# Kernel optimization log

Measured on AMD Instinct MI355X. Metric: run time of the kernel, lower is better.

## Reference

```python
import jax, jax.numpy as jnp
import numpy as np

SEQ, BATCH, IN, HID = 2048, 4096, 4, 3


def setup_inputs() -> dict:
    key = jax.random.key(0)
    ks = jax.random.split(key, 6)
    s = 1.0 / np.sqrt(HID)  # PyTorch RNN init scale
    return {
        "x": jax.random.normal(ks[0], (SEQ, BATCH, IN), dtype=jnp.float32),
        "h0": jax.random.normal(ks[1], (1, BATCH, HID), dtype=jnp.float32),
        "W_ih": jax.random.uniform(ks[2], (HID, IN), minval=-s, maxval=s, dtype=jnp.float32),
        "W_hh": jax.random.uniform(ks[3], (HID, HID), minval=-s, maxval=s, dtype=jnp.float32),
        "b_ih": jax.random.uniform(ks[4], (HID,), minval=-s, maxval=s, dtype=jnp.float32),
        "b_hh": jax.random.uniform(ks[5], (HID,), minval=-s, maxval=s, dtype=jnp.float32),
    }


def reference(x, h0, W_ih, W_hh, b_ih, b_hh):
    # Single-layer ReLU RNN (batch_first=False):
    #   h_t = relu(x_t @ W_ih^T + b_ih + h_{t-1} @ W_hh^T + b_hh)
    # Precompute the input projection for all timesteps (vectorized GEMM),
    # then scan only the tiny recurrent update.
    pre = jnp.einsum('tbi,hi->tbh', x, W_ih) + b_ih + b_hh  # [T,B,H]

    def step(h, pre_t):
        h_new = jax.nn.relu(pre_t + h @ W_hh.T)  # [B,H]
        return h_new, h_new

    h_last, outs = jax.lax.scan(step, h0[0], pre)
    return outs, h_last[None]  # ([T,B,H], [1,B,H]) as nn.RNN returns
```

## Files before the change

kernel.cpp:

```cpp
#include <hip/hip_runtime.h>

#define T_SEQ   2048
#define BATCH   4096
#define BPB     16
#define NBLK    (BATCH / BPB)
#define CHUNK   64
#define NCHUNK  (T_SEQ / CHUNK)
#define XR      4
#define NS      3
#define NITER   (NCHUNK + 1)

typedef float v4f __attribute__((ext_vector_type(4)));

#define AS1c(p) ((const __attribute__((address_space(1))) void*)(p))
#define AS3(p)  ((__attribute__((address_space(3))) void*)(p))

#define BARRIER() do {                              \
    __builtin_amdgcn_sched_barrier(0);              \
    asm volatile("s_barrier" ::: "memory");         \
    __builtin_amdgcn_sched_barrier(0);              \
} while (0)

#define QBCAST(hf, pat) \
    __builtin_bit_cast(float, __builtin_amdgcn_mov_dpp( \
        __builtin_bit_cast(int, (hf)), (pat), 0xF, 0xF, true))

__global__ __launch_bounds__(256, 1) void rnn_fused(
    const float* __restrict__ x,
    const float* __restrict__ h0,
    const float* __restrict__ Wih,
    const float* __restrict__ Whh,
    const float* __restrict__ bih,
    const float* __restrict__ bhh,
    float* __restrict__ out)
{
    __shared__ v4f xs[XR * CHUNK * BPB];

    const int tid  = threadIdx.x;
    const int lane = tid & 63;
    const int wid  = tid >> 6;
    const int b0   = blockIdx.x * BPB;

    if (wid > 0) {
        const int s = wid - 1;
        const v4f* __restrict__ xg = (const v4f*)x;
        const int vlo = (lane >> 4) * BATCH + b0 + (lane & 15);

#define STAGE(c) do {                                                          \
        const int _slot = ((c) & (XR - 1)) * (CHUNK * BPB);                    \
        _Pragma("unroll")                                                      \
        for (int _g = 0; _g < CHUNK / 4; ++_g) {                               \
            __builtin_amdgcn_global_load_lds(                                  \
                AS1c(xg + ((size_t)(c) * CHUNK + _g * 4) * BATCH + vlo),       \
                AS3(&xs[_slot + _g * (4 * BPB)]), 16, 0, 0);                   \
        }                                                                      \
    } while (0)

        if (s == 0) STAGE(0);
        if (s == 1) STAGE(1);
#pragma unroll 1
        for (int i = 0; i < NITER; ++i) {
            const int ci = i + 2;
            if (ci < NCHUNK && (ci % NS) == s) STAGE(ci);
            if (i < NCHUNK && (i % NS) == s)
                asm volatile("s_waitcnt vmcnt(0)" ::: "memory");
            BARRIER();
        }
#undef STAGE
    } else {
        const int bi = lane >> 2;
        const int j  = lane & 3;
        const int jj = (j < 3) ? j : 2;

        const float w0 = Wih[jj * 4 + 0], w1 = Wih[jj * 4 + 1];
        const float w2 = Wih[jj * 4 + 2], w3 = Wih[jj * 4 + 3];
        const float a0 = Whh[jj * 3 + 0], a1 = Whh[jj * 3 + 1];
        const float a2 = Whh[jj * 3 + 2];
        const float bb = bih[jj] + bhh[jj];

        float h = h0[(b0 + bi) * 3 + jj];
        const size_t ooff = (size_t)(b0 + bi) * 3 + j;

#pragma unroll 1
        for (int i = 0; i < NITER; ++i) {
            const int c = i - 1;
            if (c >= 0 && j < 3) {
                const v4f* __restrict__ xr = &xs[(c & (XR - 1)) * (CHUNK * BPB) + bi];
                float* __restrict__ op = out + (size_t)c * CHUNK * (BATCH * 3) + ooff;
#pragma unroll
                for (int tt = 0; tt < CHUNK; ++tt) {
                    v4f xv = xr[tt * BPB];
                    float p = fmaf(w0, xv.x, fmaf(w1, xv.y,
                              fmaf(w2, xv.z, fmaf(w3, xv.w, bb))));
                    float g0 = QBCAST(h, 0x00);
                    float g1 = QBCAST(h, 0x55);
                    float g2 = QBCAST(h, 0xAA);
                    float t0 = fmaf(a0, g0, fmaf(a1, g1, fmaf(a2, g2, p)));
                    h = fmaxf(t0, 0.0f);
                    op[(size_t)tt * (BATCH * 3)] = h;
                }
            }
            BARRIER();
        }
        if (j < 3)
            out[(size_t)T_SEQ * BATCH * 3 + ooff] = h;
    }
}

extern "C" void kernel_launch(void* const* d_in, const int* in_sizes, int n_in,
                              void* d_out, int out_size, void* d_ws, size_t ws_size,
                              hipStream_t stream) {
    const float* x   = (const float*)d_in[0];
    const float* h0  = (const float*)d_in[1];
    const float* Wih = (const float*)d_in[2];
    const float* Whh = (const float*)d_in[3];
    const float* bih = (const float*)d_in[4];
    const float* bhh = (const float*)d_in[5];
    float* out = (float*)d_out;

    rnn_fused<<<NBLK, 256, 0, stream>>>(x, h0, Wih, Whh, bih, bhh, out);
}
```

Measured before the change: 250.7 us.

## Split RNN into projection, recurrence, and store warps with deeper LDS pipeline

Adds a dedicated wavefront that computes the input projection into an LDS buffer, and another that copies recurrent outputs from LDS to global memory with coalesced 16-byte stores. This leaves the serial recurrence wave with only the DPP broadcast, three FMAs and an LDS write per step, with prefetched projection values. The block grows to 384 threads, the pipeline gets two more stages, and more LDS and barriers are used.

```diff
diff --git a/kernel.cpp b/kernel.cpp
--- a/kernel.cpp
+++ b/kernel.cpp
@@ -7,8 +7,10 @@
 #define CHUNK   64
 #define NCHUNK  (T_SEQ / CHUNK)
 #define XR      4
+#define NP      2
+#define NO      2
 #define NS      3
-#define NITER   (NCHUNK + 1)
+#define NITER   (NCHUNK + 3)
 
 typedef float v4f __attribute__((ext_vector_type(4)));
 
@@ -21,11 +23,13 @@
     __builtin_amdgcn_sched_barrier(0);              \
 } while (0)
 
+#define LGKM0() asm volatile("s_waitcnt lgkmcnt(0)" ::: "memory")
+
 #define QBCAST(hf, pat) \
     __builtin_bit_cast(float, __builtin_amdgcn_mov_dpp( \
         __builtin_bit_cast(int, (hf)), (pat), 0xF, 0xF, true))
 
-__global__ __launch_bounds__(256, 1) void rnn_fused(
+__global__ __launch_bounds__(384, 1) void rnn_fused(
     const float* __restrict__ x,
     const float* __restrict__ h0,
     const float* __restrict__ Wih,
@@ -34,25 +38,27 @@
     const float* __restrict__ bhh,
     float* __restrict__ out)
 {
-    __shared__ v4f xs[XR * CHUNK * BPB];
+    __shared__ v4f  xs[XR * CHUNK * BPB];
+    __shared__ v4f  ps[NP * CHUNK * BPB];
+    __shared__ float hs[NO * CHUNK * 48];
 
     const int tid  = threadIdx.x;
     const int lane = tid & 63;
     const int wid  = tid >> 6;
     const int b0   = blockIdx.x * BPB;
 
-    if (wid > 0) {
-        const int s = wid - 1;
+    if (wid >= 2 && wid <= 4) {
+        const int s = wid - 2;
         const v4f* __restrict__ xg = (const v4f*)x;
         const int vlo = (lane >> 4) * BATCH + b0 + (lane & 15);
 
 #define STAGE(c) do {                                                          \
-        const int _slot = ((c) & (XR - 1)) * (CHUNK * BPB);                    \
+        const int _s0 = ((c) & (XR - 1)) * (CHUNK * BPB);                      \
         _Pragma("unroll")                                                      \
         for (int _g = 0; _g < CHUNK / 4; ++_g) {                               \
             __builtin_amdgcn_global_load_lds(                                  \
                 AS1c(xg + ((size_t)(c) * CHUNK + _g * 4) * BATCH + vlo),       \
-                AS3(&xs[_slot + _g * (4 * BPB)]), 16, 0, 0);                   \
+                AS3(&xs[_s0 + _g * (4 * BPB)]), 16, 0, 0);                     \
         }                                                                      \
     } while (0)
 
@@ -67,43 +73,101 @@
             BARRIER();
         }
 #undef STAGE
-    } else {
+    } else if (wid == 1) {
+        const int ts = lane >> 4;
+        const int bi = lane & 15;
+        const float w00 = Wih[0], w01 = Wih[1], w02 = Wih[2],  w03 = Wih[3];
+        const float w10 = Wih[4], w11 = Wih[5], w12 = Wih[6],  w13 = Wih[7];
+        const float w20 = Wih[8], w21 = Wih[9], w22 = Wih[10], w23 = Wih[11];
+        const float bb0 = bih[0] + bhh[0];
+        const float bb1 = bih[1] + bhh[1];
+        const float bb2 = bih[2] + bhh[2];
+#pragma unroll 1
+        for (int i = 0; i < NITER; ++i) {
+            const int c = i - 1;
+            if (c >= 0 && c < NCHUNK) {
+                const v4f* __restrict__ xb = &xs[((c & (XR - 1)) * CHUNK + ts) * BPB + bi];
+                v4f* __restrict__ pw = &ps[((c & (NP - 1)) * CHUNK + ts) * BPB + bi];
+                v4f xa = xb[0];
+                v4f xc = xb[64];
+#pragma unroll
+                for (int g = 0; g < 16; ++g) {
+                    v4f xv = xa; xa = xc;
+                    xc = xb[(g + 2) * 64];
+                    float p0 = fmaf(w00, xv.x, fmaf(w01, xv.y,
+                               fmaf(w02, xv.z, fmaf(w03, xv.w, bb0))));
+                    float p1 = fmaf(w10, xv.x, fmaf(w11, xv.y,
+                               fmaf(w12, xv.z, fmaf(w13, xv.w, bb1))));
+                    float p2 = fmaf(w20, xv.x, fmaf(w21, xv.y,
+                               fmaf(w22, xv.z, fmaf(w23, xv.w, bb2))));
+                    v4f pv; pv.x = p0; pv.y = p1; pv.z = p2; pv.w = p2;
+                    pw[g * 64] = pv;
+                }
+                LGKM0();
+            }
+            BARRIER();
+        }
+    } else if (wid == 0) {
         const int bi = lane >> 2;
         const int j  = lane & 3;
         const int jj = (j < 3) ? j : 2;
-
-        const float w0 = Wih[jj * 4 + 0], w1 = Wih[jj * 4 + 1];
-        const float w2 = Wih[jj * 4 + 2], w3 = Wih[jj * 4 + 3];
-        const float a0 = Whh[jj * 3 + 0], a1 = Whh[jj * 3 + 1];
-        const float a2 = Whh[jj * 3 + 2];
-        const float bb = bih[jj] + bhh[jj];
-
+        const float a0 = Whh[jj * 3 + 0], a1 = Whh[jj * 3 + 1], a2 = Whh[jj * 3 + 2];
         float h = h0[(b0 + bi) * 3 + jj];
-        const size_t ooff = (size_t)(b0 + bi) * 3 + j;
 
 #pragma unroll 1
         for (int i = 0; i < NITER; ++i) {
-            const int c = i - 1;
-            if (c >= 0 && j < 3) {
-                const v4f* __restrict__ xr = &xs[(c & (XR - 1)) * (CHUNK * BPB) + bi];
-                float* __restrict__ op = out + (size_t)c * CHUNK * (BATCH * 3) + ooff;
+            const int c = i - 2;
+            if (c >= 0 && c < NCHUNK && j < 3) {
+                const float* __restrict__ pb =
+                    (const float*)&ps[(c & (NP - 1)) * CHUNK * BPB] + bi * 4 + jj;
+                float* __restrict__ hb = &hs[(c & (NO - 1)) * CHUNK * 48 + bi * 3 + j];
+                float q0 = pb[0 * 64], q1 = pb[1 * 64], q2 = pb[2 * 64], q3 = pb[3 * 64];
+                float q4 = pb[4 * 64], q5 = pb[5 * 64], q6 = pb[6 * 64], q7 = pb[7 * 64];
+#define STEPC(TT, Q) do {                                                      \
+                float g2 = QBCAST(h, 0xAA);                                    \
+                float g1 = QBCAST(h, 0x55);                                    \
+                float g0 = QBCAST(h, 0x00);                                    \
+                float t0 = fmaf(a0, g0, fmaf(a1, g1, fmaf(a2, g2, (Q))));      \
+                h = fmaxf(t0, 0.0f);                                           \
+                hb[(TT) * 48] = h;                                             \
+                Q = pb[((TT) + 8) * 64];                                       \
+            } while (0)
 #pragma unroll
-                for (int tt = 0; tt < CHUNK; ++tt) {
-                    v4f xv = xr[tt * BPB];
-                    float p = fmaf(w0, xv.x, fmaf(w1, xv.y,
-                              fmaf(w2, xv.z, fmaf(w3, xv.w, bb))));
-                    float g0 = QBCAST(h, 0x00);
-                    float g1 = QBCAST(h, 0x55);
-                    float g2 = QBCAST(h, 0xAA);
-                    float t0 = fmaf(a0, g0, fmaf(a1, g1, fmaf(a2, g2, p)));
-                    h = fmaxf(t0, 0.0f);
-                    op[(size_t)tt * (BATCH * 3)] = h;
+                for (int t8 = 0; t8 < CHUNK; t8 += 8) {
+                    STEPC(t8 + 0, q0); STEPC(t8 + 1, q1);
+                    STEPC(t8 + 2, q2); STEPC(t8 + 3, q3);
+                    STEPC(t8 + 4, q4); STEPC(t8 + 5, q5);
+                    STEPC(t8 + 6, q6); STEPC(t8 + 7, q7);
                 }
+#undef STEPC
+                LGKM0();
             }
             BARRIER();
         }
         if (j < 3)
-            out[(size_t)T_SEQ * BATCH * 3 + ooff] = h;
+            out[(size_t)T_SEQ * BATCH * 3 + (size_t)(b0 + bi) * 3 + j] = h;
+    } else {
+        unsigned lt = (unsigned)(lane * 4) / 48;
+        unsigned r  = (unsigned)(lane * 4) - lt * 48;
+#pragma unroll 1
+        for (int i = 0; i < NITER; ++i) {
+            const int c = i - 3;
+            if (c >= 0 && c < NCHUNK) {
+                const float* __restrict__ hb = &hs[(c & (NO - 1)) * CHUNK * 48];
+                char* __restrict__ oc = (char*)(out + (size_t)c * CHUNK * (BATCH * 3)
+                                                + (size_t)b0 * 3);
+                unsigned ltw = lt, rw = r;
+#pragma unroll
+                for (int w = 0; w < 12; ++w) {
+                    v4f v = *(const v4f*)&hb[w * 256 + lane * 4];
+                    *(v4f*)(oc + (size_t)ltw * (BATCH * 3 * 4) + rw * 4) = v;
+                    rw += 16; ltw += 5;
+                    if (rw >= 48) { rw -= 48; ltw += 1; }
+                }
+                LGKM0();
+            }
+            BARRIER();
+        }
     }
 }
 
@@ -118,5 +182,5 @@
     const float* bhh = (const float*)d_in[5];
     float* out = (float*)d_out;
 
-    rnn_fused<<<NBLK, 256, 0, stream>>>(x, h0, Wih, Whh, bih, bhh, out);
+    rnn_fused<<<NBLK, 384, 0, stream>>>(x, h0, Wih, Whh, bih, bhh, out);
 }
```

Result: faster. 237.9 us (-5.1%).
